# Kernel tuning notes

Hardware: AMD Instinct MI355X
Metric: run time of the kernel (lower is better)

Reference implementation:

```python
import jax, jax.numpy as jnp
import numpy as np

B, S, D, H = 2, 2048, 2048, 16
HD = D // H  # 128


def _rope_tables(seq_len, dim, base=10000.0):
    inv_freq = 1.0 / (base ** (jnp.arange(0, dim, 2, dtype=jnp.float32) / dim))
    t = jnp.arange(seq_len, dtype=jnp.float32)
    freqs = jnp.outer(t, inv_freq)  # [S, dim/2]
    return jnp.cos(freqs), jnp.sin(freqs)


def _apply_rotary(x, cos, sin):
    # x: [B, S, H, HD]; cos/sin: [S, HD/2] -> broadcast [1, S, 1, HD/2]
    half = x.shape[-1] // 2
    x1, x2 = x[..., :half], x[..., half:]
    c = cos[None, :, None, :]
    s = sin[None, :, None, :]
    return jnp.concatenate([x1 * c - x2 * s, x1 * s + x2 * c], axis=-1)


def setup_inputs() -> dict:
    key = jax.random.key(0)
    ks = jax.random.split(key, 5)
    x = jax.random.normal(ks[0], (B, S, D), dtype=jnp.float32)
    Wq = jax.random.normal(ks[1], (D, D), dtype=jnp.float32) * 0.02
    Wk = jax.random.normal(ks[2], (D, D), dtype=jnp.float32) * 0.02
    Wv = jax.random.normal(ks[3], (D, D), dtype=jnp.float32) * 0.02
    Wo = jax.random.normal(ks[4], (D, D), dtype=jnp.float32) * 0.02
    mask = jnp.tril(jnp.ones((S, S), dtype=jnp.int32))[None, None]  # [1,1,S,S] causal
    return {"x": x, "mask": mask, "Wq": Wq, "Wk": Wk, "Wv": Wv, "Wo": Wo}


def reference(x, mask, Wq, Wk, Wv, Wo):
    b, s, d = x.shape
    # nn.Linear(bias=False): y = x @ W.T
    q = (x @ Wq.T).reshape(b, s, H, HD)
    k = (x @ Wk.T).reshape(b, s, H, HD)
    v = (x @ Wv.T).reshape(b, s, H, HD)
    cos, sin = _rope_tables(s, HD)
    q = _apply_rotary(q, cos, sin)
    k = _apply_rotary(k, cos, sin)
    # -> [B, H, S, HD]
    q = q.transpose(0, 2, 1, 3)
    k = k.transpose(0, 2, 1, 3)
    v = v.transpose(0, 2, 1, 3)
    scores = jnp.einsum('bhqd,bhkd->bhqk', q, k) / jnp.sqrt(jnp.float32(HD))
    scores = jnp.where(mask == 0, -jnp.inf, scores)
    attn = jax.nn.softmax(scores, axis=-1)
    out = jnp.einsum('bhqk,bhkd->bhqd', attn, v)
    out = out.transpose(0, 2, 1, 3).reshape(b, s, d)
    return out @ Wo.T
```

## Files before the change

kernel.cpp:

```cpp
#include <hip/hip_runtime.h>
#include <hip/hip_bf16.h>

typedef __attribute__((ext_vector_type(8))) short short8;
typedef __attribute__((ext_vector_type(4))) short s4;
typedef __attribute__((ext_vector_type(4))) float f32x4;

#define S_TOK 2048

__device__ __forceinline__ float b2f(ushort u) {
  union { unsigned i; float f; } v; v.i = ((unsigned)u) << 16; return v.f;
}
__device__ __forceinline__ ushort f2b(float f) {
  __hip_bfloat16 h = __float2bfloat16(f);
  union { __hip_bfloat16 h; ushort u; } v; v.h = h; return v.u;
}

__device__ __forceinline__ void async_load16(const void* g, void* l) {
  __builtin_amdgcn_global_load_lds(
      (const __attribute__((address_space(1))) unsigned int*)g,
      (__attribute__((address_space(3))) unsigned int*)l, 16, 0, 0);
}

__device__ __forceinline__ void wg_barrier() {
  __asm__ volatile("" ::: "memory");
  __builtin_amdgcn_s_barrier();
  __asm__ volatile("" ::: "memory");
}

__device__ const int QT_OF[40] = {0,1,2,3, 4,4,5,5,6,6,7,7, 8,8,8,9,9,9,10,10,10,11,11,11,
                                  12,12,12,12,13,13,13,13,14,14,14,14,15,15,15,15};
__device__ const int C_OF[40]  = {0,0,0,0, 0,1,0,1,0,1,0,1, 0,1,2,0,1,2,0,1,2,0,1,2,
                                  0,1,2,3,0,1,2,3,0,1,2,3,0,1,2,3};
__device__ const int S0_OF[16] = {0,1,2,3,4,6,8,10,12,15,18,21,24,28,32,36};
__device__ const int NC_OF[16] = {1,1,1,1,2,2,2,2,3,3,3,3,4,4,4,4};

__global__ __launch_bounds__(256) void cvt_f32_bf16(const float* __restrict__ in,
                                                    ushort* __restrict__ out, int n) {
  int i = (blockIdx.x * 256 + threadIdx.x) * 4;
  if (i < n) {
    float4 v = *(const float4*)(in + i);
    ushort4 o;
    o.x = f2b(v.x); o.y = f2b(v.y); o.z = f2b(v.z); o.w = f2b(v.w);
    *(ushort4*)(out + i) = o;
  }
}

__global__ __launch_bounds__(256) void cvt_w4(const float* __restrict__ w0,
                                              const float* __restrict__ w1,
                                              const float* __restrict__ w2,
                                              const float* __restrict__ w3,
                                              ushort* __restrict__ out, int n) {
  const float* src = blockIdx.y == 0 ? w0 : blockIdx.y == 1 ? w1 : blockIdx.y == 2 ? w2 : w3;
  int i = (blockIdx.x * 256 + threadIdx.x) * 4;
  if (i < n) {
    float4 v = *(const float4*)(src + i);
    ushort4 o;
    o.x = f2b(v.x); o.y = f2b(v.y); o.z = f2b(v.z); o.w = f2b(v.w);
    *(ushort4*)(out + (size_t)blockIdx.y * n + i) = o;
  }
}

template <bool OUTF32>
__global__ __launch_bounds__(512, 2) void gemm256(const ushort* __restrict__ A,
                                                  const ushort* __restrict__ Bw,
                                                  void* __restrict__ Cv,
                                                  int lda, int ldb, int ldc) {
  __shared__ __align__(16) ushort As[4][256 * 32];
  __shared__ __align__(16) ushort Bs[4][256 * 32];
  const int tid  = threadIdx.x;
  const int lane = tid & 63;
  const int w    = tid >> 6;
  const int quad = lane >> 4;
  const int l15  = lane & 15;
  const int m0 = blockIdx.x * 256;
  const int n0 = blockIdx.y * 256;
  const int wm = (w & 1) * 128;
  const int wn = (w >> 1) * 64;

  f32x4 acc[8][4];
  #pragma unroll
  for (int i = 0; i < 8; ++i)
    #pragma unroll
    for (int j = 0; j < 4; ++j) acc[i][j] = (f32x4){0.f, 0.f, 0.f, 0.f};

  auto stage = [&](int t, int j) {
    const int r = t & 3;
    const int s = tid + j * 512;
    const int row = s >> 2, qp = s & 3;
    const int kof = (qp ^ ((row >> 1) & 3)) * 8;
    const int k0 = t * 32;
    async_load16(A  + (size_t)(m0 + row) * lda + k0 + kof, &As[r][s * 8]);
    async_load16(Bw + (size_t)(n0 + row) * ldb + k0 + kof, &Bs[r][s * 8]);
  };

  stage(0, 0); stage(0, 1);
  stage(1, 0); stage(1, 1);
  stage(2, 0); stage(2, 1);
  __asm__ volatile("s_waitcnt vmcnt(8)" ::: "memory");
  wg_barrier();

  constexpr int nT = 64;
  #pragma unroll 1
  for (int u = 0; u < nT; ++u) {
    const ushort* At = As[u & 3];
    const ushort* Bt = Bs[u & 3];
    short8 afr[4], bfr[4];

    #pragma unroll
    for (int ni = 0; ni < 4; ++ni) {
      int row = wn + ni * 16 + l15;
      bfr[ni] = *(const short8*)&Bt[(row * 4 + (quad ^ ((row >> 1) & 3))) * 8];
    }
    #pragma unroll
    for (int mi = 0; mi < 4; ++mi) {
      int row = wm + mi * 16 + l15;
      afr[mi] = *(const short8*)&At[(row * 4 + (quad ^ ((row >> 1) & 3))) * 8];
    }
    if (u + 3 < nT) stage(u + 3, 0);
    wg_barrier();
    __asm__ volatile("s_waitcnt lgkmcnt(0)" ::: "memory");
    __builtin_amdgcn_s_setprio(1);
    #pragma unroll
    for (int mi = 0; mi < 4; ++mi)
      #pragma unroll
      for (int ni = 0; ni < 4; ++ni)
        acc[mi][ni] = __builtin_amdgcn_mfma_f32_16x16x32_bf16(afr[mi], bfr[ni], acc[mi][ni], 0, 0, 0);
    __builtin_amdgcn_s_setprio(0);
    wg_barrier();

    #pragma unroll
    for (int mi = 0; mi < 4; ++mi) {
      int row = wm + 64 + mi * 16 + l15;
      afr[mi] = *(const short8*)&At[(row * 4 + (quad ^ ((row >> 1) & 3))) * 8];
    }
    if (u + 3 < nT) stage(u + 3, 1);
    wg_barrier();
    __asm__ volatile("s_waitcnt lgkmcnt(0)" ::: "memory");
    __builtin_amdgcn_s_setprio(1);
    #pragma unroll
    for (int mi = 0; mi < 4; ++mi)
      #pragma unroll
      for (int ni = 0; ni < 4; ++ni)
        acc[4 + mi][ni] = __builtin_amdgcn_mfma_f32_16x16x32_bf16(afr[mi], bfr[ni], acc[4 + mi][ni], 0, 0, 0);
    __builtin_amdgcn_s_setprio(0);
    if (u + 3 < nT)      { __asm__ volatile("s_waitcnt vmcnt(8)" ::: "memory"); }
    else if (u + 2 < nT) { __asm__ volatile("s_waitcnt vmcnt(4)" ::: "memory"); }
    else if (u + 1 < nT) { __asm__ volatile("s_waitcnt vmcnt(0)" ::: "memory"); }
    wg_barrier();
  }

  #pragma unroll
  for (int mi = 0; mi < 8; ++mi)
    #pragma unroll
    for (int ni = 0; ni < 4; ++ni)
      #pragma unroll
      for (int r = 0; r < 4; ++r) {
        int rr = m0 + wm + mi * 16 + quad * 4 + r;
        int cc = n0 + wn + ni * 16 + l15;
        if constexpr (OUTF32)
          ((float*)Cv)[(size_t)rr * ldc + cc] = acc[mi][ni][r];
        else
          ((ushort*)Cv)[(size_t)rr * ldc + cc] = f2b(acc[mi][ni][r]);
      }
}

__global__ __launch_bounds__(256) void rope_k(ushort* __restrict__ QK) {
  const int t = blockIdx.x * 256 + threadIdx.x;
  const int j = t & 63;
  const int h = (t >> 6) & 15;
  const int row = t >> 10;
  const int pos = row & (S_TOK - 1);
  const float invf = __expf(-0.14391156831212787f * (float)j);
  const float ph = (float)pos * invf;
  float sn, cs;
  __sincosf(ph, &sn, &cs);
  size_t base = (size_t)row * 4096 + h * 128 + j;
  float x1 = b2f(QK[base]);
  float x2 = b2f(QK[base + 64]);
  QK[base]      = f2b(x1 * cs - x2 * sn);
  QK[base + 64] = f2b(x1 * sn + x2 * cs);
  float y1 = b2f(QK[base + 2048]);
  float y2 = b2f(QK[base + 2048 + 64]);
  QK[base + 2048]      = f2b(y1 * cs - y2 * sn);
  QK[base + 2048 + 64] = f2b(y1 * sn + y2 * cs);
}

__global__ __launch_bounds__(256, 2) void attn_chunk(const ushort* __restrict__ QK,
                                                     const ushort* __restrict__ Vt,
                                                     ushort* __restrict__ Opart,
                                                     float* __restrict__ Ml) {
  __shared__ __align__(16) ushort Ks[2][8192];
  __shared__ __align__(16) ushort Vs[2][8192];
  const int s = blockIdx.x, h = blockIdx.y, b = blockIdx.z;
  const int qt = QT_OF[s], c = C_OF[s];
  const int q0 = qt * 128;
  const int t0 = c * 8, tend = min(t0 + 8, 2 * qt + 2);
  const int slot = (b * 16 + h) * 40 + s;
  const int tid = threadIdx.x, lane = tid & 63, w = tid >> 6;
  const int quad = lane >> 4, l15 = lane & 15;
  const size_t rowbase = (size_t)b * S_TOK;
  const float scale = 0.08838834764831845f;

  short8 qf[2][4];
  #pragma unroll
  for (int m = 0; m < 2; ++m)
    #pragma unroll
    for (int ks = 0; ks < 4; ++ks)
      qf[m][ks] = *(const short8*)(QK + (rowbase + q0 + w * 32 + m * 16 + l15) * 4096
                                   + h * 128 + ks * 32 + quad * 8);

  f32x4 o[2][8];
  #pragma unroll
  for (int m = 0; m < 2; ++m)
    #pragma unroll
    for (int no = 0; no < 8; ++no) o[m][no] = (f32x4){0.f, 0.f, 0.f, 0.f};
  float lsum[2] = {0.f, 0.f};

  auto issue_k = [&](int t, int buf) {
    const ushort* kb = QK + (rowbase + (size_t)t * 64) * 4096 + 2048 + h * 128;
    #pragma unroll
    for (int i = 0; i < 4; ++i) {
      int sl = tid + i * 256;
      int row = sl >> 4, cs = sl & 15;
      async_load16(kb + (size_t)row * 4096 + (cs ^ (row & 15)) * 8, &Ks[buf][sl * 8]);
    }
  };
  auto issue_v = [&](int t, int buf) {
    const ushort* vb = Vt + (size_t)(h * 128) * 4096 + b * S_TOK + (size_t)t * 64;
    #pragma unroll
    for (int i = 0; i < 4; ++i) {
      int sl = tid + i * 256;
      int hd = sl >> 3, cc = (sl & 7) ^ (hd & 7);
      async_load16(vb + (size_t)hd * 4096 + cc * 8, &Vs[buf][sl * 8]);
    }
  };

  issue_k(t0, 0);
  issue_v(t0, 0);

  for (int t = t0; t < tend; ++t) {
    const int buf = (t - t0) & 1;
    __syncthreads();
    if (t + 1 < tend) { issue_k(t + 1, buf ^ 1); issue_v(t + 1, buf ^ 1); }

    const ushort* KsT = Ks[buf];
    const ushort* VsT = Vs[buf];
    const bool domask = (t * 64 + 64 > q0);

    #pragma unroll
    for (int n = 0; n < 4; ++n) {
      short8 kf[4];
      #pragma unroll
      for (int ks = 0; ks < 4; ++ks) {
        int row = n * 16 + l15;
        kf[ks] = *(const short8*)&KsT[(row * 16 + ((ks * 4 + quad) ^ (row & 15))) * 8];
      }
      s4 pfm[2];
      #pragma unroll
      for (int m = 0; m < 2; ++m) {
        f32x4 z = (f32x4){0.f, 0.f, 0.f, 0.f};
        #pragma unroll
        for (int ks = 0; ks < 4; ++ks)
          z = __builtin_amdgcn_mfma_f32_16x16x32_bf16(kf[ks], qf[m][ks], z, 0, 0, 0);
        const int qg = q0 + w * 32 + m * 16 + l15;
        float p[4];
        #pragma unroll
        for (int r = 0; r < 4; ++r) {
          int kvg = t * 64 + n * 16 + quad * 4 + r;
          float pv = __expf(z[r] * scale);
          if (domask && kvg > qg) pv = 0.f;
          p[r] = pv;
          lsum[m] += pv;
        }
        s4 pk;
        pk[0] = (short)f2b(p[0]); pk[1] = (short)f2b(p[1]);
        pk[2] = (short)f2b(p[2]); pk[3] = (short)f2b(p[3]);
        pfm[m] = pk;
      }
      #pragma unroll
      for (int no = 0; no < 8; ++no) {
        int hd = no * 16 + l15;
        int cc = 2 * n + (quad >> 1);
        s4 vf = *(const s4*)&VsT[(hd * 8 + (cc ^ (hd & 7))) * 8 + (quad & 1) * 4];
        #pragma unroll
        for (int m = 0; m < 2; ++m)
          o[m][no] = __builtin_amdgcn_mfma_f32_16x16x16bf16_1k(pfm[m], vf, o[m][no], 0, 0, 0);
      }
    }
  }

  #pragma unroll
  for (int m = 0; m < 2; ++m) {
    lsum[m] += __shfl_xor(lsum[m], 16);
    lsum[m] += __shfl_xor(lsum[m], 32);
  }
  if (quad == 0) {
    #pragma unroll
    for (int m = 0; m < 2; ++m)
      Ml[(size_t)slot * 128 + w * 32 + m * 16 + l15] = lsum[m];
  }

  __syncthreads();
  ushort* Es = &Ks[0][w * 2048];
  ushort* Op = Opart + (size_t)slot * 16384;
  #pragma unroll
  for (int m = 0; m < 2; ++m) {
    #pragma unroll
    for (int no = 0; no < 8; ++no)
      #pragma unroll
      for (int r = 0; r < 4; ++r)
        Es[(quad * 4 + r) * 128 + no * 16 + l15] = f2b(o[m][no][r]);
    __asm__ volatile("s_waitcnt lgkmcnt(0)" ::: "memory");
    #pragma unroll
    for (int j = 0; j < 4; ++j) {
      int cchunk = lane * 4 + j;
      int row_l = cchunk >> 4, colc = cchunk & 15;
      short8 vv = *(const short8*)&Es[row_l * 128 + colc * 8];
      *(short8*)(Op + (size_t)(w * 32 + m * 16 + row_l) * 128 + colc * 8) = vv;
    }
    __asm__ volatile("s_waitcnt lgkmcnt(0)" ::: "memory");
  }
}

__global__ __launch_bounds__(256) void attn_combine(const ushort* __restrict__ Opart,
                                                    const float* __restrict__ Ml,
                                                    ushort* __restrict__ Ob) {
  const int qt = blockIdx.x, h = blockIdx.y, b = blockIdx.z;
  const int nc = NC_OF[qt];
  const int base = (b * 16 + h) * 40 + S0_OF[qt];
  const int tid = threadIdx.x;
  const int row = tid >> 1, half = tid & 1;

  float l = 0.f;
  for (int c = 0; c < nc; ++c) l += Ml[(size_t)(base + c) * 128 + row];
  const float inv_l = 1.f / l;

  float acc[64];
  #pragma unroll
  for (int i = 0; i < 64; ++i) acc[i] = 0.f;
  for (int c = 0; c < nc; ++c) {
    const ushort* Op = Opart + (size_t)(base + c) * 16384 + row * 128 + half * 64;
    #pragma unroll
    for (int k = 0; k < 8; ++k) {
      short8 v = *(const short8*)(Op + k * 8);
      #pragma unroll
      for (int u = 0; u < 8; ++u) acc[k * 8 + u] += b2f((ushort)v[u]);
    }
  }

  ushort* dst = Ob + ((size_t)(b * S_TOK + qt * 128 + row)) * 2048 + h * 128 + half * 64;
  #pragma unroll
  for (int k = 0; k < 8; ++k) {
    short8 ov;
    #pragma unroll
    for (int u = 0; u < 8; ++u) ov[u] = (short)f2b(acc[k * 8 + u] * inv_l);
    *(short8*)(dst + k * 8) = ov;
  }
}

extern "C" void kernel_launch(void* const* d_in, const int* in_sizes, int n_in,
                              void* d_out, int out_size, void* d_ws, size_t ws_size,
                              hipStream_t stream) {
  const float* x  = (const float*)d_in[0];
  const float* Wq = (const float*)d_in[2];
  const float* Wk = (const float*)d_in[3];
  const float* Wv = (const float*)d_in[4];
  const float* Wo = (const float*)d_in[5];
  float* out = (float*)d_out;

  ushort* xb    = (ushort*)d_ws;
  ushort* Wb    = xb + (size_t)4096 * 2048;
  ushort* QK    = Wb + (size_t)4 * 2048 * 2048;
  ushort* Vt    = QK + (size_t)4096 * 4096;
  ushort* Opart = Vt + (size_t)2048 * 4096;
  float*  Ml    = (float*)(Opart + (size_t)1280 * 16384);
  ushort* Ob    = xb;

  const int NX = 4096 * 2048;
  const int NW = 2048 * 2048;
  dim3 blk(256);
  dim3 blk512(512);

  cvt_f32_bf16<<<dim3(NX / 1024), blk, 0, stream>>>(x, xb, NX);
  cvt_w4<<<dim3(NW / 1024, 4), blk, 0, stream>>>(Wq, Wk, Wv, Wo, Wb, NW);

  gemm256<false><<<dim3(16, 16), blk512, 0, stream>>>(xb, Wb, QK, 2048, 2048, 4096);
  gemm256<false><<<dim3(8, 16), blk512, 0, stream>>>(Wb + (size_t)2 * NW, xb, Vt, 2048, 2048, 4096);
  rope_k<<<dim3(16384), blk, 0, stream>>>(QK);
  attn_chunk<<<dim3(40, 16, 2), blk, 0, stream>>>(QK, Vt, Opart, Ml);
  attn_combine<<<dim3(16, 16, 2), blk, 0, stream>>>(Opart, Ml, Ob);
  gemm256<true><<<dim3(16, 8), blk512, 0, stream>>>(Ob, Wb + (size_t)3 * NW, out, 2048, 2048, 2048);
}
```

Baseline: 446.8 us.

## Use smaller GEMM tiles for V/O projections, reorder attention chunks, swizzle epilogue

```diff
diff --git a/kernel.cpp b/kernel.cpp
--- a/kernel.cpp
+++ b/kernel.cpp
@@ -33,6 +33,8 @@
                                   0,1,2,3,0,1,2,3,0,1,2,3,0,1,2,3};
 __device__ const int S0_OF[16] = {0,1,2,3,4,6,8,10,12,15,18,21,24,28,32,36};
 __device__ const int NC_OF[16] = {1,1,1,1,2,2,2,2,3,3,3,3,4,4,4,4};
+__device__ const int SORD[40] = {3,4,6,8,10,11,12,13,15,16,18,19,21,22,23,24,25,26,28,29,
+                                 30,32,33,34,36,37,38,39, 2,9,20,35, 1,7,17,31, 0,5,14,27};
 
 __global__ __launch_bounds__(256) void cvt_f32_bf16(const float* __restrict__ in,
                                                     ushort* __restrict__ out, int n) {
@@ -153,6 +155,104 @@
   for (int mi = 0; mi < 8; ++mi)
     #pragma unroll
     for (int ni = 0; ni < 4; ++ni)
+      #pragma unroll
+      for (int r = 0; r < 4; ++r) {
+        int rr = m0 + wm + mi * 16 + quad * 4 + r;
+        int cc = n0 + wn + ni * 16 + l15;
+        if constexpr (OUTF32)
+          ((float*)Cv)[(size_t)rr * ldc + cc] = acc[mi][ni][r];
+        else
+          ((ushort*)Cv)[(size_t)rr * ldc + cc] = f2b(acc[mi][ni][r]);
+      }
+}
+
+template <int BM, int BN, bool OUTF32>
+__global__ __launch_bounds__(512, 2) void gemm_mn(const ushort* __restrict__ A,
+                                                  const ushort* __restrict__ Bw,
+                                                  void* __restrict__ Cv,
+                                                  int lda, int ldb, int ldc) {
+  constexpr int LA = BM / 128;
+  constexpr int LB = BN / 128;
+  constexpr int MI = BM / 32;
+  constexpr int NI = BN / 64;
+  static_assert(LA + LB == 3, "vmcnt literals assume 3 loads/thread/tile");
+  __shared__ __align__(16) ushort As[4][BM * 32];
+  __shared__ __align__(16) ushort Bs[4][BN * 32];
+  const int tid  = threadIdx.x;
+  const int lane = tid & 63;
+  const int w    = tid >> 6;
+  const int quad = lane >> 4;
+  const int l15  = lane & 15;
+  const int m0 = blockIdx.x * BM;
+  const int n0 = blockIdx.y * BN;
+  const int wm = (w & 1) * (BM / 2);
+  const int wn = (w >> 1) * (BN / 4);
+
+  f32x4 acc[MI][NI];
+  #pragma unroll
+  for (int i = 0; i < MI; ++i)
+    #pragma unroll
+    for (int j = 0; j < NI; ++j) acc[i][j] = (f32x4){0.f, 0.f, 0.f, 0.f};
+
+  auto stage = [&](int t) {
+    const int r = t & 3;
+    const int k0 = t * 32;
+    #pragma unroll
+    for (int ja = 0; ja < LA; ++ja) {
+      int s = tid + ja * 512;
+      int row = s >> 2, qp = s & 3;
+      int kof = (qp ^ ((row >> 1) & 3)) * 8;
+      async_load16(A + (size_t)(m0 + row) * lda + k0 + kof, &As[r][s * 8]);
+    }
+    #pragma unroll
+    for (int jb = 0; jb < LB; ++jb) {
+      int s = tid + jb * 512;
+      int row = s >> 2, qp = s & 3;
+      int kof = (qp ^ ((row >> 1) & 3)) * 8;
+      async_load16(Bw + (size_t)(n0 + row) * ldb + k0 + kof, &Bs[r][s * 8]);
+    }
+  };
+
+  stage(0); stage(1); stage(2);
+  __asm__ volatile("s_waitcnt vmcnt(6)" ::: "memory");
+  wg_barrier();
+
+  constexpr int nT = 64;
+  #pragma unroll 1
+  for (int u = 0; u < nT; ++u) {
+    const ushort* At = As[u & 3];
+    const ushort* Bt = Bs[u & 3];
+    short8 afr[MI], bfr[NI];
+    #pragma unroll
+    for (int ni = 0; ni < NI; ++ni) {
+      int row = wn + ni * 16 + l15;
+      bfr[ni] = *(const short8*)&Bt[(row * 4 + (quad ^ ((row >> 1) & 3))) * 8];
+    }
+    #pragma unroll
+    for (int mi = 0; mi < MI; ++mi) {
+      int row = wm + mi * 16 + l15;
+      afr[mi] = *(const short8*)&At[(row * 4 + (quad ^ ((row >> 1) & 3))) * 8];
+    }
+    if (u + 3 < nT) stage(u + 3);
+    wg_barrier();
+    __asm__ volatile("s_waitcnt lgkmcnt(0)" ::: "memory");
+    __builtin_amdgcn_s_setprio(1);
+    #pragma unroll
+    for (int mi = 0; mi < MI; ++mi)
+      #pragma unroll
+      for (int ni = 0; ni < NI; ++ni)
+        acc[mi][ni] = __builtin_amdgcn_mfma_f32_16x16x32_bf16(afr[mi], bfr[ni], acc[mi][ni], 0, 0, 0);
+    __builtin_amdgcn_s_setprio(0);
+    if (u + 3 < nT)      { __asm__ volatile("s_waitcnt vmcnt(6)" ::: "memory"); }
+    else if (u + 2 < nT) { __asm__ volatile("s_waitcnt vmcnt(3)" ::: "memory"); }
+    else if (u + 1 < nT) { __asm__ volatile("s_waitcnt vmcnt(0)" ::: "memory"); }
+    wg_barrier();
+  }
+
+  #pragma unroll
+  for (int mi = 0; mi < MI; ++mi)
+    #pragma unroll
+    for (int ni = 0; ni < NI; ++ni)
       #pragma unroll
       for (int r = 0; r < 4; ++r) {
         int rr = m0 + wm + mi * 16 + quad * 4 + r;
@@ -191,7 +291,8 @@
                                                      float* __restrict__ Ml) {
   __shared__ __align__(16) ushort Ks[2][8192];
   __shared__ __align__(16) ushort Vs[2][8192];
-  const int s = blockIdx.x, h = blockIdx.y, b = blockIdx.z;
+  const int s = SORD[blockIdx.x];
+  const int h = blockIdx.y, b = blockIdx.z;
   const int qt = QT_OF[s], c = C_OF[s];
   const int q0 = qt * 128;
   const int t0 = c * 8, tend = min(t0 + 8, 2 * qt + 2);
@@ -199,7 +300,7 @@
   const int tid = threadIdx.x, lane = tid & 63, w = tid >> 6;
   const int quad = lane >> 4, l15 = lane & 15;
   const size_t rowbase = (size_t)b * S_TOK;
-  const float scale = 0.08838834764831845f;
+  const float kSc2 = 0.12751743f;
 
   short8 qf[2][4];
   #pragma unroll
@@ -267,7 +368,7 @@
         #pragma unroll
         for (int r = 0; r < 4; ++r) {
           int kvg = t * 64 + n * 16 + quad * 4 + r;
-          float pv = __expf(z[r] * scale);
+          float pv = exp2f(z[r] * kSc2);
           if (domask && kvg > qg) pv = 0.f;
           p[r] = pv;
           lsum[m] += pv;
@@ -308,14 +409,17 @@
     #pragma unroll
     for (int no = 0; no < 8; ++no)
       #pragma unroll
-      for (int r = 0; r < 4; ++r)
-        Es[(quad * 4 + r) * 128 + no * 16 + l15] = f2b(o[m][no][r]);
+      for (int r = 0; r < 4; ++r) {
+        int rr = quad * 4 + r;
+        int c8 = (no * 2 + (l15 >> 3)) ^ (rr & 7);
+        Es[rr * 128 + c8 * 8 + (l15 & 7)] = f2b(o[m][no][r]);
+      }
     __asm__ volatile("s_waitcnt lgkmcnt(0)" ::: "memory");
     #pragma unroll
     for (int j = 0; j < 4; ++j) {
       int cchunk = lane * 4 + j;
       int row_l = cchunk >> 4, colc = cchunk & 15;
-      short8 vv = *(const short8*)&Es[row_l * 128 + colc * 8];
+      short8 vv = *(const short8*)&Es[row_l * 128 + (colc ^ (row_l & 7)) * 8];
       *(short8*)(Op + (size_t)(w * 32 + m * 16 + row_l) * 128 + colc * 8) = vv;
     }
     __asm__ volatile("s_waitcnt lgkmcnt(0)" ::: "memory");
@@ -385,9 +489,11 @@
   cvt_w4<<<dim3(NW / 1024, 4), blk, 0, stream>>>(Wq, Wk, Wv, Wo, Wb, NW);
 
   gemm256<false><<<dim3(16, 16), blk512, 0, stream>>>(xb, Wb, QK, 2048, 2048, 4096);
-  gemm256<false><<<dim3(8, 16), blk512, 0, stream>>>(Wb + (size_t)2 * NW, xb, Vt, 2048, 2048, 4096);
+  gemm_mn<128, 256, false><<<dim3(16, 16), blk512, 0, stream>>>(Wb + (size_t)2 * NW, xb, Vt,
+                                                                2048, 2048, 4096);
   rope_k<<<dim3(16384), blk, 0, stream>>>(QK);
   attn_chunk<<<dim3(40, 16, 2), blk, 0, stream>>>(QK, Vt, Opart, Ml);
   attn_combine<<<dim3(16, 16, 2), blk, 0, stream>>>(Opart, Ml, Ob);
-  gemm256<true><<<dim3(16, 8), blk512, 0, stream>>>(Ob, Wb + (size_t)3 * NW, out, 2048, 2048, 2048);
-}
+  gemm_mn<256, 128, true><<<dim3(16, 16), blk512, 0, stream>>>(Ob, Wb + (size_t)3 * NW, out,
+                                                               2048, 2048, 2048);
+}
```

After: 413.7 us. 7.4% less time.

## Rework GEMM tiling, fuse Q rope into attention, reorder chunks, swizzle epilogue

Applied to the files above, without the earlier changes.

```diff
diff --git a/kernel.cpp b/kernel.cpp
--- a/kernel.cpp
+++ b/kernel.cpp
@@ -33,6 +33,8 @@
                                   0,1,2,3,0,1,2,3,0,1,2,3,0,1,2,3};
 __device__ const int S0_OF[16] = {0,1,2,3,4,6,8,10,12,15,18,21,24,28,32,36};
 __device__ const int NC_OF[16] = {1,1,1,1,2,2,2,2,3,3,3,3,4,4,4,4};
+__device__ const int SORD[40] = {3,4,6,8,10,11,12,13,15,16,18,19,21,22,23,24,25,26,28,29,
+                                 30,32,33,34,36,37,38,39, 2,9,20,35, 1,7,17,31, 0,5,14,27};
 
 __global__ __launch_bounds__(256) void cvt_f32_bf16(const float* __restrict__ in,
                                                     ushort* __restrict__ out, int n) {
@@ -60,99 +62,102 @@
   }
 }
 
-template <bool OUTF32>
-__global__ __launch_bounds__(512, 2) void gemm256(const ushort* __restrict__ A,
+template <int BM, int BN, bool OUTF32>
+__global__ __launch_bounds__(512, 1) void gemm_v2(const ushort* __restrict__ A,
                                                   const ushort* __restrict__ Bw,
                                                   void* __restrict__ Cv,
                                                   int lda, int ldb, int ldc) {
-  __shared__ __align__(16) ushort As[4][256 * 32];
-  __shared__ __align__(16) ushort Bs[4][256 * 32];
+  constexpr int MI = BM / 32;
+  constexpr int NI = BN / 64;
+  constexpr int JA = BM / 64;
+  constexpr int JB = BN / 64;
+  __shared__ __align__(16) ushort As[2][BM * 64];
+  __shared__ __align__(16) ushort Bs[2][BN * 64];
   const int tid  = threadIdx.x;
   const int lane = tid & 63;
   const int w    = tid >> 6;
   const int quad = lane >> 4;
   const int l15  = lane & 15;
-  const int m0 = blockIdx.x * 256;
-  const int n0 = blockIdx.y * 256;
-  const int wm = (w & 1) * 128;
-  const int wn = (w >> 1) * 64;
-
-  f32x4 acc[8][4];
-  #pragma unroll
-  for (int i = 0; i < 8; ++i)
-    #pragma unroll
-    for (int j = 0; j < 4; ++j) acc[i][j] = (f32x4){0.f, 0.f, 0.f, 0.f};
-
-  auto stage = [&](int t, int j) {
-    const int r = t & 3;
-    const int s = tid + j * 512;
-    const int row = s >> 2, qp = s & 3;
-    const int kof = (qp ^ ((row >> 1) & 3)) * 8;
-    const int k0 = t * 32;
-    async_load16(A  + (size_t)(m0 + row) * lda + k0 + kof, &As[r][s * 8]);
-    async_load16(Bw + (size_t)(n0 + row) * ldb + k0 + kof, &Bs[r][s * 8]);
+  const int m0 = blockIdx.x * BM;
+  const int n0 = blockIdx.y * BN;
+  const int wm = (w & 1) * (BM / 2);
+  const int wn = (w >> 1) * (BN / 4);
+
+  f32x4 acc[MI][NI];
+  #pragma unroll
+  for (int i = 0; i < MI; ++i)
+    #pragma unroll
+    for (int j = 0; j < NI; ++j) acc[i][j] = (f32x4){0.f, 0.f, 0.f, 0.f};
+
+  auto stage = [&](int t) {
+    const int rb = t & 1;
+    const int k0 = t * 64;
+    #pragma unroll
+    for (int j = 0; j < JA; ++j) {
+      int s2 = tid + j * 512;
+      int row = s2 >> 3, c = s2 & 7;
+      async_load16(A + (size_t)(m0 + row) * lda + k0 + (c ^ (row & 7)) * 8,
+                   &As[rb][s2 * 8]);
+    }
+    #pragma unroll
+    for (int j = 0; j < JB; ++j) {
+      int s2 = tid + j * 512;
+      int row = s2 >> 3, c = s2 & 7;
+      async_load16(Bw + (size_t)(n0 + row) * ldb + k0 + (c ^ (row & 7)) * 8,
+                   &Bs[rb][s2 * 8]);
+    }
   };
 
-  stage(0, 0); stage(0, 1);
-  stage(1, 0); stage(1, 1);
-  stage(2, 0); stage(2, 1);
-  __asm__ volatile("s_waitcnt vmcnt(8)" ::: "memory");
+  stage(0);
+  __asm__ volatile("s_waitcnt vmcnt(0)" ::: "memory");
   wg_barrier();
 
-  constexpr int nT = 64;
+  constexpr int nT = 32;
   #pragma unroll 1
-  for (int u = 0; u < nT; ++u) {
-    const ushort* At = As[u & 3];
-    const ushort* Bt = Bs[u & 3];
-    short8 afr[4], bfr[4];
-
-    #pragma unroll
-    for (int ni = 0; ni < 4; ++ni) {
-      int row = wn + ni * 16 + l15;
-      bfr[ni] = *(const short8*)&Bt[(row * 4 + (quad ^ ((row >> 1) & 3))) * 8];
-    }
-    #pragma unroll
-    for (int mi = 0; mi < 4; ++mi) {
-      int row = wm + mi * 16 + l15;
-      afr[mi] = *(const short8*)&At[(row * 4 + (quad ^ ((row >> 1) & 3))) * 8];
-    }
-    if (u + 3 < nT) stage(u + 3, 0);
-    wg_barrier();
-    __asm__ volatile("s_waitcnt lgkmcnt(0)" ::: "memory");
-    __builtin_amdgcn_s_setprio(1);
-    #pragma unroll
-    for (int mi = 0; mi < 4; ++mi)
-      #pragma unroll
-      for (int ni = 0; ni < 4; ++ni)
-        acc[mi][ni] = __builtin_amdgcn_mfma_f32_16x16x32_bf16(afr[mi], bfr[ni], acc[mi][ni], 0, 0, 0);
-    __builtin_amdgcn_s_setprio(0);
-    wg_barrier();
-
-    #pragma unroll
-    for (int mi = 0; mi < 4; ++mi) {
-      int row = wm + 64 + mi * 16 + l15;
-      afr[mi] = *(const short8*)&At[(row * 4 + (quad ^ ((row >> 1) & 3))) * 8];
-    }
-    if (u + 3 < nT) stage(u + 3, 1);
-    wg_barrier();
-    __asm__ volatile("s_waitcnt lgkmcnt(0)" ::: "memory");
-    __builtin_amdgcn_s_setprio(1);
-    #pragma unroll
-    for (int mi = 0; mi < 4; ++mi)
-      #pragma unroll
-      for (int ni = 0; ni < 4; ++ni)
-        acc[4 + mi][ni] = __builtin_amdgcn_mfma_f32_16x16x32_bf16(afr[mi], bfr[ni], acc[4 + mi][ni], 0, 0, 0);
-    __builtin_amdgcn_s_setprio(0);
-    if (u + 3 < nT)      { __asm__ volatile("s_waitcnt vmcnt(8)" ::: "memory"); }
-    else if (u + 2 < nT) { __asm__ volatile("s_waitcnt vmcnt(4)" ::: "memory"); }
-    else if (u + 1 < nT) { __asm__ volatile("s_waitcnt vmcnt(0)" ::: "memory"); }
-    wg_barrier();
-  }
-
-  #pragma unroll
-  for (int mi = 0; mi < 8; ++mi)
-    #pragma unroll
-    for (int ni = 0; ni < 4; ++ni)
+  for (int t = 0; t < nT; ++t) {
+    const ushort* At = As[t & 1];
+    const ushort* Bt = Bs[t & 1];
+    if (t + 1 < nT) stage(t + 1);
+
+    short8 afr[MI][2];
+    #pragma unroll
+    for (int mi = 0; mi < MI; ++mi)
+      #pragma unroll
+      for (int kk = 0; kk < 2; ++kk) {
+        int rg = wm + mi * 16 + l15;
+        int ch = (kk * 4 + quad) ^ (rg & 7);
+        afr[mi][kk] = *(const short8*)&At[rg * 64 + ch * 8];
+      }
+
+    #pragma unroll
+    for (int ni = 0; ni < NI; ++ni) {
+      short8 bfr[2];
+      #pragma unroll
+      for (int kk = 0; kk < 2; ++kk) {
+        int rg = wn + ni * 16 + l15;
+        int ch = (kk * 4 + quad) ^ (rg & 7);
+        bfr[kk] = *(const short8*)&Bt[rg * 64 + ch * 8];
+      }
+      __builtin_amdgcn_s_setprio(1);
+      #pragma unroll
+      for (int mi = 0; mi < MI; ++mi)
+        #pragma unroll
+        for (int kk = 0; kk < 2; ++kk)
+          acc[mi][ni] = __builtin_amdgcn_mfma_f32_16x16x32_bf16(afr[mi][kk], bfr[kk],
+                                                                acc[mi][ni], 0, 0, 0);
+      __builtin_amdgcn_s_setprio(0);
+    }
+
+    if (t + 1 < nT) {
+      __asm__ volatile("s_waitcnt vmcnt(0)" ::: "memory");
+      wg_barrier();
+    }
+  }
+
+  #pragma unroll
+  for (int mi = 0; mi < MI; ++mi)
+    #pragma unroll
+    for (int ni = 0; ni < NI; ++ni)
       #pragma unroll
       for (int r = 0; r < 4; ++r) {
         int rr = m0 + wm + mi * 16 + quad * 4 + r;
@@ -174,15 +179,11 @@
   const float ph = (float)pos * invf;
   float sn, cs;
   __sincosf(ph, &sn, &cs);
-  size_t base = (size_t)row * 4096 + h * 128 + j;
-  float x1 = b2f(QK[base]);
-  float x2 = b2f(QK[base + 64]);
-  QK[base]      = f2b(x1 * cs - x2 * sn);
-  QK[base + 64] = f2b(x1 * sn + x2 * cs);
-  float y1 = b2f(QK[base + 2048]);
-  float y2 = b2f(QK[base + 2048 + 64]);
-  QK[base + 2048]      = f2b(y1 * cs - y2 * sn);
-  QK[base + 2048 + 64] = f2b(y1 * sn + y2 * cs);
+  size_t base = (size_t)row * 4096 + 2048 + h * 128 + j;
+  float y1 = b2f(QK[base]);
+  float y2 = b2f(QK[base + 64]);
+  QK[base]      = f2b(y1 * cs - y2 * sn);
+  QK[base + 64] = f2b(y1 * sn + y2 * cs);
 }
 
 __global__ __launch_bounds__(256, 2) void attn_chunk(const ushort* __restrict__ QK,
@@ -191,7 +192,8 @@
                                                      float* __restrict__ Ml) {
   __shared__ __align__(16) ushort Ks[2][8192];
   __shared__ __align__(16) ushort Vs[2][8192];
-  const int s = blockIdx.x, h = blockIdx.y, b = blockIdx.z;
+  const int s = SORD[blockIdx.x];
+  const int h = blockIdx.y, b = blockIdx.z;
   const int qt = QT_OF[s], c = C_OF[s];
   const int q0 = qt * 128;
   const int t0 = c * 8, tend = min(t0 + 8, 2 * qt + 2);
@@ -208,6 +210,24 @@
     for (int ks = 0; ks < 4; ++ks)
       qf[m][ks] = *(const short8*)(QK + (rowbase + q0 + w * 32 + m * 16 + l15) * 4096
                                    + h * 128 + ks * 32 + quad * 8);
+
+  #pragma unroll
+  for (int m = 0; m < 2; ++m) {
+    const int pos = (q0 + w * 32 + m * 16 + l15) & (S_TOK - 1);
+    #pragma unroll
+    for (int ks = 0; ks < 2; ++ks)
+      #pragma unroll
+      for (int j = 0; j < 8; ++j) {
+        const int dj = ks * 32 + quad * 8 + j;
+        const float ph = (float)pos * __expf(-0.14391156831212787f * (float)dj);
+        float sn, cs;
+        __sincosf(ph, &sn, &cs);
+        const float x1 = b2f((ushort)qf[m][ks][j]);
+        const float x2 = b2f((ushort)qf[m][ks + 2][j]);
+        qf[m][ks][j]     = (short)f2b(x1 * cs - x2 * sn);
+        qf[m][ks + 2][j] = (short)f2b(x1 * sn + x2 * cs);
+      }
+  }
 
   f32x4 o[2][8];
   #pragma unroll
@@ -308,14 +328,17 @@
     #pragma unroll
     for (int no = 0; no < 8; ++no)
       #pragma unroll
-      for (int r = 0; r < 4; ++r)
-        Es[(quad * 4 + r) * 128 + no * 16 + l15] = f2b(o[m][no][r]);
+      for (int r = 0; r < 4; ++r) {
+        int rr = quad * 4 + r;
+        int c8 = (no * 2 + (l15 >> 3)) ^ (rr & 7);
+        Es[rr * 128 + c8 * 8 + (l15 & 7)] = f2b(o[m][no][r]);
+      }
     __asm__ volatile("s_waitcnt lgkmcnt(0)" ::: "memory");
     #pragma unroll
     for (int j = 0; j < 4; ++j) {
       int cchunk = lane * 4 + j;
       int row_l = cchunk >> 4, colc = cchunk & 15;
-      short8 vv = *(const short8*)&Es[row_l * 128 + colc * 8];
+      short8 vv = *(const short8*)&Es[row_l * 128 + (colc ^ (row_l & 7)) * 8];
       *(short8*)(Op + (size_t)(w * 32 + m * 16 + row_l) * 128 + colc * 8) = vv;
     }
     __asm__ volatile("s_waitcnt lgkmcnt(0)" ::: "memory");
@@ -384,10 +407,12 @@
   cvt_f32_bf16<<<dim3(NX / 1024), blk, 0, stream>>>(x, xb, NX);
   cvt_w4<<<dim3(NW / 1024, 4), blk, 0, stream>>>(Wq, Wk, Wv, Wo, Wb, NW);
 
-  gemm256<false><<<dim3(16, 16), blk512, 0, stream>>>(xb, Wb, QK, 2048, 2048, 4096);
-  gemm256<false><<<dim3(8, 16), blk512, 0, stream>>>(Wb + (size_t)2 * NW, xb, Vt, 2048, 2048, 4096);
+  gemm_v2<256, 256, false><<<dim3(16, 16), blk512, 0, stream>>>(xb, Wb, QK, 2048, 2048, 4096);
+  gemm_v2<128, 256, false><<<dim3(16, 16), blk512, 0, stream>>>(Wb + (size_t)2 * NW, xb, Vt,
+                                                                2048, 2048, 4096);
   rope_k<<<dim3(16384), blk, 0, stream>>>(QK);
   attn_chunk<<<dim3(40, 16, 2), blk, 0, stream>>>(QK, Vt, Opart, Ml);
   attn_combine<<<dim3(16, 16, 2), blk, 0, stream>>>(Opart, Ml, Ob);
-  gemm256<true><<<dim3(16, 8), blk512, 0, stream>>>(Ob, Wb + (size_t)3 * NW, out, 2048, 2048, 2048);
-}
+  gemm_v2<256, 128, true><<<dim3(16, 16), blk512, 0, stream>>>(Ob, Wb + (size_t)3 * NW, out,
+                                                               2048, 2048, 2048);
+}
```

Result: faster. 418.7 us (-6.3%).
